# Performance work log

Hardware: AMD Instinct MI355X
Metric: run time of the kernel (lower is better)

Reference implementation:

```python
import jax, jax.numpy as jnp
import numpy as np

N_NODES = 100000
N_EDGES = 1600000
N_GRAPHS = 64
F_IN = 256
HID = 256
PROJ = 128
L = 4


def setup_inputs() -> dict:
    key = jax.random.key(0)
    ks = jax.random.split(key, 12)
    x = jax.random.normal(ks[0], (N_NODES, F_IN), dtype=jnp.float32)
    edge_index = jax.random.randint(ks[1], (2, N_EDGES), 0, N_NODES)
    batch = jnp.sort(jax.random.randint(ks[2], (N_NODES,), 0, N_GRAPHS))
    s = 0.05
    # SAGEConv per layer: lin_l (applied to mean-aggregated neighbors, with bias)
    # and lin_r (applied to root node, no bias). All layers are 256->256, stacked.
    Wl = jax.random.normal(ks[3], (L, HID, HID), dtype=jnp.float32) * s
    bl = jax.random.normal(ks[4], (L, HID), dtype=jnp.float32) * s
    Wr = jax.random.normal(ks[5], (L, HID, HID), dtype=jnp.float32) * s
    gamma = jnp.ones((L, HID), dtype=jnp.float32)
    beta = jnp.zeros((L, HID), dtype=jnp.float32)
    W1 = jax.random.normal(ks[6], (HID, HID), dtype=jnp.float32) * s
    b1 = jnp.zeros((HID,), dtype=jnp.float32)
    W2 = jax.random.normal(ks[7], (HID, PROJ), dtype=jnp.float32) * s
    b2 = jnp.zeros((PROJ,), dtype=jnp.float32)
    return {"x": x, "edge_index": edge_index, "batch": batch,
            "Wl": Wl, "bl": bl, "Wr": Wr, "gamma": gamma, "beta": beta,
            "W1": W1, "b1": b1, "W2": W2, "b2": b2}


def _segment_mean(vals, seg_ids, num_segments):
    sums = jax.ops.segment_sum(vals, seg_ids, num_segments=num_segments)
    cnt = jax.ops.segment_sum(jnp.ones((vals.shape[0],), vals.dtype), seg_ids,
                              num_segments=num_segments)
    return sums / jnp.maximum(cnt, 1.0)[:, None]


def reference(x, edge_index, batch, Wl, bl, Wr, gamma, beta, W1, b1, W2, b2):
    src, dst = edge_index[0], edge_index[1]
    eps = 1e-5
    h = x
    for i in range(L):
        # SAGEConv: mean-aggregate neighbor features, then lin_l(aggr) + lin_r(root)
        aggr = _segment_mean(h[src], dst, N_NODES)          # [N, HID]
        h = aggr @ Wl[i] + bl[i] + h @ Wr[i]
        # BatchNorm1d (training-mode batch statistics, biased variance)
        mu = jnp.mean(h, axis=0)
        var = jnp.mean(jnp.square(h - mu), axis=0)
        h = (h - mu) * jax.lax.rsqrt(var + eps) * gamma[i] + beta[i]
        h = jax.nn.relu(h)
        # dropout omitted (inference / deterministic reference)
    g = _segment_mean(h, batch, N_GRAPHS)                   # [G, HID]
    z = jax.nn.relu(g @ W1 + b1) @ W2 + b2                  # [G, PROJ]
    # F.normalize(z, dim=1): L2 normalize with eps clamp
    norm = jnp.maximum(jnp.linalg.norm(z, axis=1, keepdims=True), 1e-12)
    return z / norm
```

## Files before the change

kernel.cpp:

```cpp
#include <hip/hip_runtime.h>

#define N_NODES 100000
#define M_PAD   100096
#define N_MBLK  782
#define N_EDGES 1600000
#define N_GRAPHS 64
#define HID 256
#define PROJ 128
#define NLAYERS 4

#define EBUF_STRIDE 8192
#define N_BUCKETS ((N_NODES + 255) / 256)
#define CSR_BLK 1024
#define EPT 10
#define CSR_NBLK ((N_EDGES + CSR_BLK * EPT - 1) / (CSR_BLK * EPT))
#define BFILL_PAD 16

typedef unsigned short u16;
typedef __attribute__((ext_vector_type(8))) short bf16x8;
typedef __attribute__((ext_vector_type(4))) float f32x4;
typedef __attribute__((ext_vector_type(2))) float vf2;

__device__ __forceinline__ float b2f(u16 u) {
  return __uint_as_float(((unsigned)u) << 16);
}
__device__ __forceinline__ float b2f_lo(unsigned u) {
  return __uint_as_float(u << 16);
}
__device__ __forceinline__ float b2f_hi(unsigned u) {
  return __uint_as_float(u & 0xFFFF0000u);
}
__device__ __forceinline__ u16 f2b(float f) {
  unsigned u = __float_as_uint(f);
  u = (u + 0x7FFF + ((u >> 16) & 1)) >> 16;
  return (u16)u;
}
__device__ __forceinline__ void gload16(const void* g, void* l) {
  __builtin_amdgcn_global_load_lds((const __attribute__((address_space(1))) void*)g,
                                   (__attribute__((address_space(3))) void*)l, 16, 0, 0);
}
__device__ __forceinline__ unsigned pack_fp8x4(float a, float b, float c, float d) {
  int v = __builtin_amdgcn_cvt_pk_fp8_f32(a, b, 0, false);
  v = __builtin_amdgcn_cvt_pk_fp8_f32(c, d, v, true);
  return (unsigned)v;
}
__device__ __forceinline__ void accf8(float* a, unsigned w) {
  vf2 lo = __builtin_amdgcn_cvt_pk_f32_fp8((int)w, false);
  vf2 hi = __builtin_amdgcn_cvt_pk_f32_fp8((int)w, true);
  a[0] += lo.x; a[1] += lo.y; a[2] += hi.x; a[3] += hi.y;
}

__global__ __launch_bounds__(1024) void bucket_count_scatter(
    const int* __restrict__ src, const int* __restrict__ dst,
    int* __restrict__ cnt, int* __restrict__ bfill, uint2* __restrict__ ebuf) {
  __shared__ int lhist[N_BUCKETS];
  __shared__ int lbase[N_BUCKETS];
  int t = threadIdx.x;
  int e0 = blockIdx.x * (CSR_BLK * EPT) + t;
  for (int i = t; i < N_BUCKETS; i += CSR_BLK) lhist[i] = 0;
  __syncthreads();
  int sv[EPT], dv[EPT];
#pragma unroll
  for (int j = 0; j < EPT; j++) {
    int e = e0 + j * CSR_BLK;
    if (e < N_EDGES) {
      sv[j] = src[e];
      dv[j] = dst[e];
      atomicAdd(&cnt[dv[j]], 1);
      atomicAdd(&lhist[dv[j] >> 8], 1);
    } else {
      dv[j] = -1;
      sv[j] = 0;
    }
  }
  __syncthreads();
  for (int i = t; i < N_BUCKETS; i += CSR_BLK) {
    lbase[i] = atomicAdd(&bfill[i * BFILL_PAD], lhist[i]);
    lhist[i] = 0;
  }
  __syncthreads();
#pragma unroll
  for (int j = 0; j < EPT; j++) {
    if (dv[j] >= 0) {
      int b = dv[j] >> 8;
      int p = lbase[b] + atomicAdd(&lhist[b], 1);
      if (p < EBUF_STRIDE) {
        uint2 q;
        q.x = (unsigned)sv[j];
        q.y = (unsigned)dv[j];
        ebuf[(size_t)b * EBUF_STRIDE + p] = q;
      }
    }
  }
}

__global__ void inv_kernel(const int* __restrict__ cnt, float* __restrict__ inv) {
  int n = blockIdx.x * blockDim.x + threadIdx.x;
  if (n < N_NODES) inv[n] = 1.0f / fmaxf((float)cnt[n], 1.0f);
}

#define SCAN_BLK 1024
#define N_SCAN_BLOCKS ((N_NODES + SCAN_BLK - 1) / SCAN_BLK)

__global__ __launch_bounds__(256) void scan_partial(const int* __restrict__ cnt,
                                                    int* __restrict__ bsum) {
  __shared__ int red[256];
  int t = threadIdx.x;
  int base = blockIdx.x * SCAN_BLK + t * 4;
  int s = 0;
#pragma unroll
  for (int j = 0; j < 4; j++) {
    int i = base + j;
    if (i < N_NODES) s += cnt[i];
  }
  red[t] = s;
  __syncthreads();
  for (int off = 128; off > 0; off >>= 1) {
    if (t < off) red[t] += red[t + off];
    __syncthreads();
  }
  if (t == 0) bsum[blockIdx.x] = red[0];
}

__global__ __launch_bounds__(128) void scan_bsums(const int* __restrict__ bsum,
                                                  int* __restrict__ boff) {
  __shared__ int tile[128];
  int t = threadIdx.x;
  int v = (t < N_SCAN_BLOCKS) ? bsum[t] : 0;
  tile[t] = v;
  __syncthreads();
#pragma unroll
  for (int off = 1; off < 128; off <<= 1) {
    int add = (t >= off) ? tile[t - off] : 0;
    __syncthreads();
    tile[t] += add;
    __syncthreads();
  }
  if (t < N_SCAN_BLOCKS) boff[t] = tile[t] - v;
}

__global__ __launch_bounds__(256) void scan_final(const int* __restrict__ cnt,
                                                  const int* __restrict__ boff,
                                                  int* __restrict__ row_ptr) {
  __shared__ int tsum[256];
  int t = threadIdx.x;
  int base = blockIdx.x * SCAN_BLK + t * 4;
  int v[4];
  int s = 0;
#pragma unroll
  for (int j = 0; j < 4; j++) {
    int i = base + j;
    v[j] = (i < N_NODES) ? cnt[i] : 0;
    s += v[j];
  }
  tsum[t] = s;
  __syncthreads();
#pragma unroll
  for (int off = 1; off < 256; off <<= 1) {
    int add = (t >= off) ? tsum[t - off] : 0;
    __syncthreads();
    tsum[t] += add;
    __syncthreads();
  }
  int excl = tsum[t] - s + boff[blockIdx.x];
#pragma unroll
  for (int j = 0; j < 4; j++) {
    int i = base + j;
    if (i < N_NODES) {
      row_ptr[i] = excl;
      excl += v[j];
    }
  }
  if (blockIdx.x == 0 && t == 0) row_ptr[N_NODES] = N_EDGES;
}

__global__ void fill_from_ebuf(const uint2* __restrict__ ebuf,
                               const int* __restrict__ bfill,
                               const int* __restrict__ row_ptr,
                               int* __restrict__ fill,
                               int* __restrict__ col) {
  int idx = blockIdx.x * blockDim.x + threadIdx.x;
  int b = idx >> 13;
  int sl = idx & (EBUF_STRIDE - 1);
  if (b < N_BUCKETS && sl < bfill[b * BFILL_PAD]) {
    uint2 q = ebuf[(size_t)b * EBUF_STRIDE + sl];
    int d = (int)q.y;
    int pos = row_ptr[d] + atomicAdd(&fill[d], 1);
    col[pos] = (int)q.x;
  }
}

__global__ __launch_bounds__(256) void convert_x(const float4* __restrict__ x,
                                                 ushort4* __restrict__ hb,
                                                 unsigned* __restrict__ h8) {
  int i = blockIdx.x * blockDim.x + threadIdx.x;
  float4 v = x[i];
  ushort4 o;
  o.x = f2b(v.x); o.y = f2b(v.y); o.z = f2b(v.z); o.w = f2b(v.w);
  hb[i] = o;
  h8[i] = pack_fp8x4(v.x, v.y, v.z, v.w);
}

__global__ __launch_bounds__(256) void convert_w(const float* __restrict__ Wl,
                                                 const float* __restrict__ Wr,
                                                 u16* __restrict__ Wt) {
  int idx = blockIdx.x * blockDim.x + threadIdx.x;
  int l = idx >> 17;
  int r = idx & ((1 << 17) - 1);
  int n = r >> 9;
  int k = r & 511;
  float v = (k < 256) ? Wl[(size_t)l * 65536 + k * 256 + n]
                      : Wr[(size_t)l * 65536 + (k - 256) * 256 + n];
  Wt[idx] = f2b(v);
}

__global__ __launch_bounds__(256) void aggregate_fp8(
    const unsigned char* __restrict__ h8, const int* __restrict__ row_ptr,
    const int* __restrict__ col, const float* __restrict__ inv_cnt,
    u16* __restrict__ aggr) {
  int node = blockIdx.x * 4 + (threadIdx.x >> 6);
  int lane = threadIdx.x & 63;
  int half = lane >> 5, l32 = lane & 31;
  int r0 = row_ptr[node], r1 = row_ptr[node + 1];
  float a[8] = {0.f, 0.f, 0.f, 0.f, 0.f, 0.f, 0.f, 0.f};
  int e = r0 + half;
  for (; e + 14 < r1; e += 16) {
    int s[8];
#pragma unroll
    for (int j = 0; j < 8; j++) s[j] = col[e + 2 * j];
    uint2 v[8];
#pragma unroll
    for (int j = 0; j < 8; j++)
      v[j] = *((const uint2*)(h8 + (size_t)s[j] * HID) + l32);
#pragma unroll
    for (int j = 0; j < 8; j++) { accf8(a, v[j].x); accf8(a + 4, v[j].y); }
  }
  for (; e + 6 < r1; e += 8) {
    int s0 = col[e], s1 = col[e + 2], s2 = col[e + 4], s3 = col[e + 6];
    uint2 v0 = *((const uint2*)(h8 + (size_t)s0 * HID) + l32);
    uint2 v1 = *((const uint2*)(h8 + (size_t)s1 * HID) + l32);
    uint2 v2 = *((const uint2*)(h8 + (size_t)s2 * HID) + l32);
    uint2 v3 = *((const uint2*)(h8 + (size_t)s3 * HID) + l32);
    accf8(a, v0.x); accf8(a + 4, v0.y);
    accf8(a, v1.x); accf8(a + 4, v1.y);
    accf8(a, v2.x); accf8(a + 4, v2.y);
    accf8(a, v3.x); accf8(a + 4, v3.y);
  }
  for (; e < r1; e += 2) {
    int s0 = col[e];
    uint2 v0 = *((const uint2*)(h8 + (size_t)s0 * HID) + l32);
    accf8(a, v0.x); accf8(a + 4, v0.y);
  }
#pragma unroll
  for (int j = 0; j < 8; j++) a[j] += __shfl_xor(a[j], 32, 64);
  if (half == 0) {
    float inv = inv_cnt[node];
    uint4 o;
    o.x = (unsigned)f2b(a[0] * inv) | ((unsigned)f2b(a[1] * inv) << 16);
    o.y = (unsigned)f2b(a[2] * inv) | ((unsigned)f2b(a[3] * inv) << 16);
    o.z = (unsigned)f2b(a[4] * inv) | ((unsigned)f2b(a[5] * inv) << 16);
    o.w = (unsigned)f2b(a[6] * inv) | ((unsigned)f2b(a[7] * inv) << 16);
    *((uint4*)(aggr + (size_t)node * HID) + l32) = o;
  }
}

__global__ __launch_bounds__(256, 2) void gemm_fused(
    const u16* hb, const u16* __restrict__ aggr,
    const u16* __restrict__ Bt, u16* hpre,
    float* __restrict__ psum) {
  __shared__ u16 smem[128 * 32 + 256 * 32];
  __shared__ float bns[4][8][16][2];
  u16* As = smem;
  u16* Bs = smem + 128 * 32;
  u16* ep = smem;

  int tid = threadIdx.x;
  int wid = tid >> 6, lane = tid & 63;
  int m0 = blockIdx.x * 128;
  int q = lane >> 4, c = lane & 15;
  int wm = (wid >> 1) * 64, wn = (wid & 1) * 128;

  f32x4 zero = {0.f, 0.f, 0.f, 0.f};
  f32x4 acc[4][8];
#pragma unroll
  for (int mi = 0; mi < 4; mi++)
#pragma unroll
    for (int ni = 0; ni < 8; ni++) acc[mi][ni] = zero;

  int srowA0 = wid * 32 + (lane >> 2);
  int cgA0 = (lane & 3) ^ ((srowA0 >> 1) & 3);
  int srowA1 = srowA0 + 16;
  int cgA1 = (lane & 3) ^ ((srowA1 >> 1) & 3);
  int srowB[4], cgB[4];
#pragma unroll
  for (int j = 0; j < 4; j++) {
    srowB[j] = j * 64 + wid * 16 + (lane >> 2);
    cgB[j] = (lane & 3) ^ ((srowB[j] >> 1) & 3);
  }

  int aoff[4], boff[8];
#pragma unroll
  for (int mi = 0; mi < 4; mi++) {
    int row = wm + mi * 16 + c;
    aoff[mi] = row * 32 + ((q ^ ((row >> 1) & 3)) << 3);
  }
#pragma unroll
  for (int ni = 0; ni < 8; ni++) {
    int row = wn + ni * 16 + c;
    boff[ni] = row * 32 + ((q ^ ((row >> 1) & 3)) << 3);
  }

  for (int k0 = 0; k0 < 512; k0 += 32) {
    const u16* Asrc = (k0 < 256) ? aggr : hb;
    int ksrc = k0 & 255;
    gload16(Asrc + ((size_t)(m0 + srowA0) * HID + ksrc + cgA0 * 8), &As[(wid * 32) * 32]);
    gload16(Asrc + ((size_t)(m0 + srowA1) * HID + ksrc + cgA1 * 8), &As[(wid * 32 + 16) * 32]);
#pragma unroll
    for (int j = 0; j < 4; j++)
      gload16(Bt + ((size_t)srowB[j] * 512 + k0 + cgB[j] * 8), &Bs[(j * 64 + wid * 16) * 32]);
    __syncthreads();
    bf16x8 af[4], bfr[8];
#pragma unroll
    for (int mi = 0; mi < 4; mi++) af[mi] = *(const bf16x8*)&As[aoff[mi]];
#pragma unroll
    for (int ni = 0; ni < 8; ni++) bfr[ni] = *(const bf16x8*)&Bs[boff[ni]];
#pragma unroll
    for (int mi = 0; mi < 4; mi++)
#pragma unroll
      for (int ni = 0; ni < 8; ni++)
        acc[mi][ni] = __builtin_amdgcn_mfma_f32_16x16x32_bf16(af[mi], bfr[ni],
                                                              acc[mi][ni], 0, 0, 0);
    __syncthreads();
  }

  int rh = wid >> 1;
#pragma unroll
  for (int mi = 0; mi < 4; mi++) {
#pragma unroll
    for (int r = 0; r < 4; r++) {
      int r16 = q * 4 + r;
#pragma unroll
      for (int ni = 0; ni < 8; ni++)
        ep[(rh * 16 + r16) * 256 + wn + ni * 16 + c] = f2b(acc[mi][ni][r]);
    }
    __syncthreads();
    int u = tid;
#pragma unroll
    for (int j = 0; j < 4; j++, u += 256) {
      int lr = u >> 5;
      int cu = u & 31;
      int gm = m0 + (lr >> 4) * 64 + mi * 16 + (lr & 15);
      if (gm < N_NODES)
        ((uint4*)(hpre + (size_t)gm * HID))[cu] = ((const uint4*)ep)[u];
    }
    __syncthreads();
  }

#pragma unroll
  for (int ni = 0; ni < 8; ni++) {
    float s = 0.f, s2 = 0.f;
#pragma unroll
    for (int mi = 0; mi < 4; mi++) {
#pragma unroll
      for (int r = 0; r < 4; r++) {
        int gm = m0 + wm + mi * 16 + q * 4 + r;
        float v = (gm < N_NODES) ? acc[mi][ni][r] : 0.f;
        s += v;
        s2 += v * v;
      }
    }
    s += __shfl_xor(s, 16, 64);
    s += __shfl_xor(s, 32, 64);
    s2 += __shfl_xor(s2, 16, 64);
    s2 += __shfl_xor(s2, 32, 64);
    if (q == 0) {
      bns[wid][ni][c][0] = s;
      bns[wid][ni][c][1] = s2;
    }
  }
  __syncthreads();
  {
    int wnh = tid >> 7, ni = (tid >> 4) & 7, cc = tid & 15;
    float s = bns[wnh][ni][cc][0] + bns[wnh + 2][ni][cc][0];
    float s2 = bns[wnh][ni][cc][1] + bns[wnh + 2][ni][cc][1];
    int coln = wnh * 128 + ni * 16 + cc;
    psum[(size_t)blockIdx.x * 512 + coln] = s;
    psum[(size_t)blockIdx.x * 512 + 256 + coln] = s2;
  }
}

#define BN_MID 16
__global__ __launch_bounds__(256) void bn_mid(const float* __restrict__ psum,
                                              float* __restrict__ tmp) {
  int b = blockIdx.x;
  int f = threadIdx.x;
  int mb0 = b * 49;
  int mb1 = min(mb0 + 49, N_MBLK);
  float s = 0.f, s2 = 0.f;
  for (int mb = mb0; mb < mb1; mb++) {
    s += psum[(size_t)mb * 512 + f];
    s2 += psum[(size_t)mb * 512 + 256 + f];
  }
  tmp[(size_t)b * 512 + f] = s;
  tmp[(size_t)b * 512 + 256 + f] = s2;
}

__global__ void bn_fin(const float* __restrict__ tmp,
                       const float* __restrict__ gamma,
                       const float* __restrict__ beta,
                       float* __restrict__ ss) {
  int f = threadIdx.x;
  float sum = 0.f, sq = 0.f;
#pragma unroll
  for (int b = 0; b < BN_MID; b++) {
    sum += tmp[(size_t)b * 512 + f];
    sq += tmp[(size_t)b * 512 + 256 + f];
  }
  const float invN = 1.0f / (float)N_NODES;
  float mu = sum * invN;
  float ex2 = sq * invN;
  float var = fmaxf(ex2 - mu * mu, 0.f);
  float sc = gamma[f] * rsqrtf(var + 1e-5f);
  ss[f] = sc;
  ss[HID + f] = beta[f] - mu * sc;
}

__global__ __launch_bounds__(256) void bn_apply_fused(const uint4* hpre,
                                                      const float* __restrict__ ss,
                                                      uint4* hout,
                                                      uint2* __restrict__ h8out) {
  int idx0 = blockIdx.x * blockDim.x + threadIdx.x;
  int cb = (idx0 & 31) * 8;
  float sc[8], sh[8];
#pragma unroll
  for (int j = 0; j < 8; j++) { sc[j] = ss[cb + j]; sh[j] = ss[HID + cb + j]; }
  const int total = N_NODES * 32;
  const int step = gridDim.x * blockDim.x;
  for (int i = idx0; i < total; i += step) {
    uint4 v = hpre[i];
    unsigned vv[4] = {v.x, v.y, v.z, v.w};
    unsigned o[4];
    float f[8];
#pragma unroll
    for (int j = 0; j < 4; j++) {
      float lo = fmaxf(fmaf(b2f_lo(vv[j]), sc[2 * j], sh[2 * j]), 0.f);
      float hi = fmaxf(fmaf(b2f_hi(vv[j]), sc[2 * j + 1], sh[2 * j + 1]), 0.f);
      f[2 * j] = lo;
      f[2 * j + 1] = hi;
      o[j] = (unsigned)f2b(lo) | ((unsigned)f2b(hi) << 16);
    }
    uint4 ov = {o[0], o[1], o[2], o[3]};
    hout[i] = ov;
    uint2 q;
    q.x = pack_fp8x4(f[0], f[1], f[2], f[3]);
    q.y = pack_fp8x4(f[4], f[5], f[6], f[7]);
    h8out[i] = q;
  }
}

__global__ __launch_bounds__(256) void pool_partial(
    const u16* __restrict__ hpre, const float* __restrict__ ss,
    const int* __restrict__ batch, float* __restrict__ partial) {
  __shared__ float red[256][9];
  int g = blockIdx.x;
  int i = blockIdx.y;
  int t = threadIdx.x;
  int a = 0, b = N_NODES;
  while (a < b) { int m = (a + b) >> 1; if (batch[m] < g) a = m + 1; else b = m; }
  int lo = a;
  b = N_NODES;
  while (a < b) { int m = (a + b) >> 1; if (batch[m] < g + 1) a = m + 1; else b = m; }
  int hi = a;
  int len = hi - lo;
  int clen = (len + 7) >> 3;
  int c0 = lo + i * clen;
  int c1 = min(c0 + clen, hi);

  int rs = t >> 5, cu = t & 31;
  int cb = cu * 8;
  float scv[8], shv[8];
#pragma unroll
  for (int j = 0; j < 8; j++) { scv[j] = ss[cb + j]; shv[j] = ss[HID + cb + j]; }
  float acc[8] = {0.f, 0.f, 0.f, 0.f, 0.f, 0.f, 0.f, 0.f};
  for (int r = c0 + rs; r < c1; r += 8) {
    uint4 v = *((const uint4*)(hpre + (size_t)r * HID) + cu);
    unsigned vv[4] = {v.x, v.y, v.z, v.w};
#pragma unroll
    for (int j = 0; j < 4; j++) {
      acc[2 * j]     += fmaxf(fmaf(b2f_lo(vv[j]), scv[2 * j], shv[2 * j]), 0.f);
      acc[2 * j + 1] += fmaxf(fmaf(b2f_hi(vv[j]), scv[2 * j + 1], shv[2 * j + 1]), 0.f);
    }
  }
#pragma unroll
  for (int j = 0; j < 8; j++) red[t][j] = acc[j];
  __syncthreads();
  int cc = t >> 3, j = t & 7;
  float sum = 0.f;
#pragma unroll
  for (int k = 0; k < 8; k++) sum += red[k * 32 + cc][j];
  partial[((size_t)g * 8 + i) * 256 + t] = sum;
}

__global__ __launch_bounds__(256) void pool_mlp_final(
    const float* __restrict__ partial, const int* __restrict__ batch,
    const float* __restrict__ W1, const float* __restrict__ b1,
    const float* __restrict__ W2, const float* __restrict__ b2,
    float* __restrict__ out) {
  __shared__ float gs[HID];
  __shared__ float ts[HID];
  __shared__ float rn[PROJ];
  int g = blockIdx.x;
  int t = threadIdx.x;
  int a = 0, b = N_NODES;
  while (a < b) { int m = (a + b) >> 1; if (batch[m] < g) a = m + 1; else b = m; }
  int lo = a;
  b = N_NODES;
  while (a < b) { int m = (a + b) >> 1; if (batch[m] < g + 1) a = m + 1; else b = m; }
  int len = a - lo;

  float sum = 0.f;
#pragma unroll
  for (int i = 0; i < 8; i++) sum += partial[((size_t)g * 8 + i) * 256 + t];
  float inv = 1.0f / fmaxf((float)len, 1.0f);
  gs[t] = sum * inv;
  __syncthreads();

  float s = b1[t];
  for (int k = 0; k < HID; k++) s = fmaf(gs[k], W1[(size_t)k * HID + t], s);
  ts[t] = fmaxf(s, 0.f);
  __syncthreads();
  float z = 0.f;
  if (t < PROJ) {
    z = b2[t];
    for (int k = 0; k < HID; k++) z = fmaf(ts[k], W2[(size_t)k * PROJ + t], z);
    rn[t] = z * z;
  }
  __syncthreads();
  for (int off = PROJ / 2; off > 0; off >>= 1) {
    if (t < off) rn[t] += rn[t + off];
    __syncthreads();
  }
  float norm = fmaxf(sqrtf(rn[0]), 1e-12f);
  if (t < PROJ) out[(size_t)g * PROJ + t] = z / norm;
}

extern "C" void kernel_launch(void* const* d_in, const int* in_sizes, int n_in,
                              void* d_out, int out_size, void* d_ws, size_t ws_size,
                              hipStream_t stream) {
  const float* x = (const float*)d_in[0];
  const int* ei = (const int*)d_in[1];
  const int* src = ei;
  const int* dst = ei + N_EDGES;
  const int* batch = (const int*)d_in[2];
  const float* Wl = (const float*)d_in[3];
  const float* Wr = (const float*)d_in[5];
  const float* gamma = (const float*)d_in[6];
  const float* beta = (const float*)d_in[7];
  const float* W1 = (const float*)d_in[8];
  const float* b1 = (const float*)d_in[9];
  const float* W2 = (const float*)d_in[10];
  const float* b2 = (const float*)d_in[11];
  float* out = (float*)d_out;

  char* p = (char*)d_ws;
  const size_t HB = (size_t)M_PAD * HID * sizeof(u16);
  u16* h = (u16*)p;      p += HB;
  u16* aggr = (u16*)p;   p += HB;
  unsigned char* h8 = (unsigned char*)p; p += (size_t)M_PAD * HID;
  u16* Wt = (u16*)p;     p += (size_t)NLAYERS * 512 * HID * sizeof(u16);
  int* col = (int*)p;    p += (size_t)N_EDGES * sizeof(int);
  int* row_ptr = (int*)p; p += 400016;
  float* inv_cnt = (float*)p; p += (size_t)N_NODES * sizeof(float);
  float* psum = (float*)p;    p += (size_t)N_MBLK * 512 * sizeof(float);
  float* tmp = (float*)p;     p += (size_t)BN_MID * 512 * sizeof(float);
  float* ss = (float*)p;      p += 512 * sizeof(float);
  float* partial = (float*)p; p += (size_t)N_GRAPHS * 8 * 256 * sizeof(float);
  int* bsum = (int*)p;        p += 128 * sizeof(int);
  int* boff = (int*)p;        p += 128 * sizeof(int);
  uint2* ebuf = (uint2*)p;    p += (size_t)N_BUCKETS * EBUF_STRIDE * sizeof(uint2);

  int* counts = (int*)aggr;
  int* fill = counts + N_NODES;
  int* bfill = fill + N_NODES;

  hipMemsetAsync(counts, 0,
                 (2 * (size_t)N_NODES + N_BUCKETS * BFILL_PAD) * sizeof(int), stream);
  bucket_count_scatter<<<CSR_NBLK, CSR_BLK, 0, stream>>>(src, dst, counts,
                                                         bfill, ebuf);
  inv_kernel<<<(N_NODES + 255) / 256, 256, 0, stream>>>(counts, inv_cnt);
  scan_partial<<<N_SCAN_BLOCKS, 256, 0, stream>>>(counts, bsum);
  scan_bsums<<<1, 128, 0, stream>>>(bsum, boff);
  scan_final<<<N_SCAN_BLOCKS, 256, 0, stream>>>(counts, boff, row_ptr);
  fill_from_ebuf<<<N_BUCKETS * (EBUF_STRIDE / 256), 256, 0, stream>>>(ebuf, bfill,
                                                                     row_ptr, fill, col);

  convert_x<<<N_NODES / 4, 256, 0, stream>>>((const float4*)x, (ushort4*)h,
                                             (unsigned*)h8);
  convert_w<<<(NLAYERS * 512 * HID) / 256, 256, 0, stream>>>(Wl, Wr, Wt);

  for (int l = 0; l < NLAYERS; l++) {
    aggregate_fp8<<<N_NODES / 4, 256, 0, stream>>>(h8, row_ptr, col, inv_cnt, aggr);
    gemm_fused<<<N_MBLK, 256, 0, stream>>>(h, aggr, Wt + (size_t)l * 512 * HID,
                                           h, psum);
    bn_mid<<<BN_MID, 256, 0, stream>>>(psum, tmp);
    bn_fin<<<1, 256, 0, stream>>>(tmp, gamma + (size_t)l * HID,
                                  beta + (size_t)l * HID, ss);
    if (l < NLAYERS - 1) {
      bn_apply_fused<<<2048, 256, 0, stream>>>((const uint4*)h, ss, (uint4*)h,
                                               (uint2*)h8);
    }
  }

  pool_partial<<<dim3(N_GRAPHS, 8), 256, 0, stream>>>(h, ss, batch, partial);
  pool_mlp_final<<<N_GRAPHS, 256, 0, stream>>>(partial, batch, W1, b1, W2, b2, out);
}
```

Before: 943.0 us.

## Build CSR per bucket in LDS, replacing global count/scan/fill passes

Per-node global atomics and the three-kernel global prefix scan are replaced by a two-level scheme. A packed 64-bit atomic per bucket tracks both the real edge count and a slot count rounded up to a multiple of 8, with sentinel padding written into the extra slots. One 512-thread kernel scans the bucket counts, and a per-bucket kernel then builds a node histogram, scan, row_ptr, inv_cnt and col placement in shared memory. This removes global per-node atomics and several launches. In exchange it depends on each bucket holding at most 8192 entries and on the sentinel padding being correct.

```diff
diff --git a/kernel.cpp b/kernel.cpp
--- a/kernel.cpp
+++ b/kernel.cpp
@@ -14,9 +14,10 @@
 #define CSR_BLK 1024
 #define EPT 10
 #define CSR_NBLK ((N_EDGES + CSR_BLK * EPT - 1) / (CSR_BLK * EPT))
-#define BFILL_PAD 16
+#define SENT 0xFFFFFFFFu
 
 typedef unsigned short u16;
+typedef unsigned long long u64;
 typedef __attribute__((ext_vector_type(8))) short bf16x8;
 typedef __attribute__((ext_vector_type(4))) float f32x4;
 typedef __attribute__((ext_vector_type(2))) float vf2;
@@ -50,9 +51,9 @@
   a[0] += lo.x; a[1] += lo.y; a[2] += hi.x; a[3] += hi.y;
 }
 
-__global__ __launch_bounds__(1024) void bucket_count_scatter(
+__global__ __launch_bounds__(1024) void bucket_scatter(
     const int* __restrict__ src, const int* __restrict__ dst,
-    int* __restrict__ cnt, int* __restrict__ bfill, uint2* __restrict__ ebuf) {
+    u64* __restrict__ bfill64, uint2* __restrict__ ebuf) {
   __shared__ int lhist[N_BUCKETS];
   __shared__ int lbase[N_BUCKETS];
   int t = threadIdx.x;
@@ -66,7 +67,6 @@
     if (e < N_EDGES) {
       sv[j] = src[e];
       dv[j] = dst[e];
-      atomicAdd(&cnt[dv[j]], 1);
       atomicAdd(&lhist[dv[j] >> 8], 1);
     } else {
       dv[j] = -1;
@@ -75,8 +75,22 @@
   }
   __syncthreads();
   for (int i = t; i < N_BUCKETS; i += CSR_BLK) {
-    lbase[i] = atomicAdd(&bfill[i * BFILL_PAD], lhist[i]);
-    lhist[i] = 0;
+    int c = lhist[i];
+    if (c > 0) {
+      int rounded = (c + 7) & ~7;
+      u64 old = atomicAdd(&bfill64[(size_t)i * 8],
+                          ((u64)rounded << 32) | (u64)c);
+      int base = (int)(old >> 32);
+      lbase[i] = base;
+      for (int k = c; k < rounded; k++) {
+        int p = base + k;
+        if (p < EBUF_STRIDE) {
+          uint2 q; q.x = 0; q.y = SENT;
+          ebuf[(size_t)i * EBUF_STRIDE + p] = q;
+        }
+      }
+      lhist[i] = 0;
+    }
   }
   __syncthreads();
 #pragma unroll
@@ -94,99 +108,79 @@
   }
 }
 
-__global__ void inv_kernel(const int* __restrict__ cnt, float* __restrict__ inv) {
-  int n = blockIdx.x * blockDim.x + threadIdx.x;
-  if (n < N_NODES) inv[n] = 1.0f / fmaxf((float)cnt[n], 1.0f);
-}
-
-#define SCAN_BLK 1024
-#define N_SCAN_BLOCKS ((N_NODES + SCAN_BLK - 1) / SCAN_BLK)
-
-__global__ __launch_bounds__(256) void scan_partial(const int* __restrict__ cnt,
-                                                    int* __restrict__ bsum) {
-  __shared__ int red[256];
+__global__ __launch_bounds__(512) void bucket_prefix(
+    const u64* __restrict__ bfill64, int* __restrict__ bucket_base,
+    int* __restrict__ row_ptr) {
+  __shared__ int tile[512];
   int t = threadIdx.x;
-  int base = blockIdx.x * SCAN_BLK + t * 4;
-  int s = 0;
-#pragma unroll
-  for (int j = 0; j < 4; j++) {
-    int i = base + j;
-    if (i < N_NODES) s += cnt[i];
-  }
-  red[t] = s;
-  __syncthreads();
-  for (int off = 128; off > 0; off >>= 1) {
-    if (t < off) red[t] += red[t + off];
-    __syncthreads();
-  }
-  if (t == 0) bsum[blockIdx.x] = red[0];
-}
-
-__global__ __launch_bounds__(128) void scan_bsums(const int* __restrict__ bsum,
-                                                  int* __restrict__ boff) {
-  __shared__ int tile[128];
+  int v = 0;
+  if (t < N_BUCKETS) {
+    u64 w = bfill64[(size_t)t * 8];
+    v = (int)(w & 0xFFFFFFFFull);
+    if ((int)(w >> 32) > EBUF_STRIDE) v = min(v, EBUF_STRIDE);
+  }
+  tile[t] = v;
+  __syncthreads();
+  for (int off = 1; off < 512; off <<= 1) {
+    int add = (t >= off) ? tile[t - off] : 0;
+    __syncthreads();
+    tile[t] += add;
+    __syncthreads();
+  }
+  if (t < N_BUCKETS) bucket_base[t] = tile[t] - v;
+  if (t == N_BUCKETS - 1) row_ptr[N_NODES] = tile[t];
+}
+
+__global__ __launch_bounds__(1024) void csr_build(
+    const uint2* __restrict__ ebuf, const u64* __restrict__ bfill64,
+    const int* __restrict__ bucket_base, int* __restrict__ row_ptr,
+    float* __restrict__ inv_cnt, int* __restrict__ col) {
+  __shared__ int hist[256];
+  __shared__ int nscan[256];
+  __shared__ int cursor[256];
+  int b = blockIdx.x;
   int t = threadIdx.x;
-  int v = (t < N_SCAN_BLOCKS) ? bsum[t] : 0;
-  tile[t] = v;
-  __syncthreads();
-#pragma unroll
-  for (int off = 1; off < 128; off <<= 1) {
-    int add = (t >= off) ? tile[t - off] : 0;
-    __syncthreads();
-    tile[t] += add;
-    __syncthreads();
-  }
-  if (t < N_SCAN_BLOCKS) boff[t] = tile[t] - v;
-}
-
-__global__ __launch_bounds__(256) void scan_final(const int* __restrict__ cnt,
-                                                  const int* __restrict__ boff,
-                                                  int* __restrict__ row_ptr) {
-  __shared__ int tsum[256];
-  int t = threadIdx.x;
-  int base = blockIdx.x * SCAN_BLK + t * 4;
-  int v[4];
-  int s = 0;
-#pragma unroll
-  for (int j = 0; j < 4; j++) {
-    int i = base + j;
-    v[j] = (i < N_NODES) ? cnt[i] : 0;
-    s += v[j];
-  }
-  tsum[t] = s;
-  __syncthreads();
-#pragma unroll
+  int nalloc = min((int)(bfill64[(size_t)b * 8] >> 32), EBUF_STRIDE);
+  int bbase = bucket_base[b];
+  if (t < 256) hist[t] = 0;
+  __syncthreads();
+  uint2 q[8];
+#pragma unroll
+  for (int k = 0; k < 8; k++) {
+    int i = t + k * CSR_BLK;
+    q[k].x = 0; q[k].y = SENT;
+    if (i < nalloc) {
+      q[k] = ebuf[(size_t)b * EBUF_STRIDE + i];
+      if (q[k].y != SENT) atomicAdd(&hist[q[k].y & 255], 1);
+    }
+  }
+  __syncthreads();
+  if (t < 256) nscan[t] = hist[t];
+  __syncthreads();
   for (int off = 1; off < 256; off <<= 1) {
-    int add = (t >= off) ? tsum[t - off] : 0;
-    __syncthreads();
-    tsum[t] += add;
-    __syncthreads();
-  }
-  int excl = tsum[t] - s + boff[blockIdx.x];
-#pragma unroll
-  for (int j = 0; j < 4; j++) {
-    int i = base + j;
-    if (i < N_NODES) {
-      row_ptr[i] = excl;
-      excl += v[j];
-    }
-  }
-  if (blockIdx.x == 0 && t == 0) row_ptr[N_NODES] = N_EDGES;
-}
-
-__global__ void fill_from_ebuf(const uint2* __restrict__ ebuf,
-                               const int* __restrict__ bfill,
-                               const int* __restrict__ row_ptr,
-                               int* __restrict__ fill,
-                               int* __restrict__ col) {
-  int idx = blockIdx.x * blockDim.x + threadIdx.x;
-  int b = idx >> 13;
-  int sl = idx & (EBUF_STRIDE - 1);
-  if (b < N_BUCKETS && sl < bfill[b * BFILL_PAD]) {
-    uint2 q = ebuf[(size_t)b * EBUF_STRIDE + sl];
-    int d = (int)q.y;
-    int pos = row_ptr[d] + atomicAdd(&fill[d], 1);
-    col[pos] = (int)q.x;
+    int add = 0;
+    if (t < 256 && t >= off) add = nscan[t - off];
+    __syncthreads();
+    if (t < 256) nscan[t] += add;
+    __syncthreads();
+  }
+  int nb = min(256, N_NODES - b * 256);
+  if (t < 256) {
+    int excl = nscan[t] - hist[t];
+    cursor[t] = excl;
+    if (t < nb) {
+      row_ptr[b * 256 + t] = bbase + excl;
+      inv_cnt[b * 256 + t] = 1.0f / fmaxf((float)hist[t], 1.0f);
+    }
+  }
+  __syncthreads();
+#pragma unroll
+  for (int k = 0; k < 8; k++) {
+    if (q[k].y != SENT) {
+      int l = (int)(q[k].y & 255);
+      int pos = bbase + atomicAdd(&cursor[l], 1);
+      col[pos] = (int)q[k].x;
+    }
   }
 }
 
@@ -575,24 +569,16 @@
   float* tmp = (float*)p;     p += (size_t)BN_MID * 512 * sizeof(float);
   float* ss = (float*)p;      p += 512 * sizeof(float);
   float* partial = (float*)p; p += (size_t)N_GRAPHS * 8 * 256 * sizeof(float);
-  int* bsum = (int*)p;        p += 128 * sizeof(int);
-  int* boff = (int*)p;        p += 128 * sizeof(int);
   uint2* ebuf = (uint2*)p;    p += (size_t)N_BUCKETS * EBUF_STRIDE * sizeof(uint2);
 
-  int* counts = (int*)aggr;
-  int* fill = counts + N_NODES;
-  int* bfill = fill + N_NODES;
-
-  hipMemsetAsync(counts, 0,
-                 (2 * (size_t)N_NODES + N_BUCKETS * BFILL_PAD) * sizeof(int), stream);
-  bucket_count_scatter<<<CSR_NBLK, CSR_BLK, 0, stream>>>(src, dst, counts,
-                                                         bfill, ebuf);
-  inv_kernel<<<(N_NODES + 255) / 256, 256, 0, stream>>>(counts, inv_cnt);
-  scan_partial<<<N_SCAN_BLOCKS, 256, 0, stream>>>(counts, bsum);
-  scan_bsums<<<1, 128, 0, stream>>>(bsum, boff);
-  scan_final<<<N_SCAN_BLOCKS, 256, 0, stream>>>(counts, boff, row_ptr);
-  fill_from_ebuf<<<N_BUCKETS * (EBUF_STRIDE / 256), 256, 0, stream>>>(ebuf, bfill,
-                                                                     row_ptr, fill, col);
+  u64* bfill64 = (u64*)aggr;
+  int* bucket_base = (int*)(bfill64 + (size_t)N_BUCKETS * 8);
+
+  hipMemsetAsync(bfill64, 0, (size_t)N_BUCKETS * 8 * sizeof(u64), stream);
+  bucket_scatter<<<CSR_NBLK, CSR_BLK, 0, stream>>>(src, dst, bfill64, ebuf);
+  bucket_prefix<<<1, 512, 0, stream>>>(bfill64, bucket_base, row_ptr);
+  csr_build<<<N_BUCKETS, CSR_BLK, 0, stream>>>(ebuf, bfill64, bucket_base,
+                                               row_ptr, inv_cnt, col);
 
   convert_x<<<N_NODES / 4, 256, 0, stream>>>((const float4*)x, (ushort4*)h,
                                              (unsigned*)h8);
```

New measurement: 849.3 us. 9.9% less time.
